# Kernel tuning notes

Measured on AMD Instinct MI355X. Metric: run time of the kernel, lower is better.

The kernel has to match this reference:

```python
import jax, jax.numpy as jnp
import numpy as np

N, CIN, C, L = 6144, 6, 128, 3
SIGMA = 0.3

def _ln(x, g, b, eps=1e-5):
    m = x.mean(-1, keepdims=True)
    v = x.var(-1, keepdims=True)
    return (x - m) / jnp.sqrt(v + eps) * g + b

def _cdist(a):
    n2 = jnp.sum(a * a, -1)
    d2 = n2[:, None] + n2[None, :] - 2.0 * (a @ a.T)
    return jnp.sqrt(jnp.maximum(d2, 0.0))

def setup_inputs():
    key = jax.random.key(0)
    ks = jax.random.split(key, 24)
    s = 1.0 / np.sqrt(C)
    ref = jax.random.normal(ks[0], (N, 3), dtype=jnp.float32)
    src = ref + 0.05 * jax.random.normal(ks[1], (N, 3), dtype=jnp.float32)
    return {
        "ref_keypts": ref,
        "src_keypts": src,
        "corr_feat": jax.random.normal(ks[2], (N, CIN), dtype=jnp.float32),
        "W_in": jax.random.normal(ks[3], (CIN + 6, C), dtype=jnp.float32) * (1.0 / np.sqrt(CIN + 6)),
        "b_in": jnp.zeros((C,), jnp.float32),
        "mlp_W": jax.random.normal(ks[4], (L, C, C), dtype=jnp.float32) * s,
        "mlp_b": jnp.zeros((L, C), jnp.float32),
        "mlp_g": jnp.ones((L, C), jnp.float32),
        "mlp_beta": jnp.zeros((L, C), jnp.float32),
        "Wq": jax.random.normal(ks[5], (L, C, C), dtype=jnp.float32) * s,
        "bq": jnp.zeros((L, C), jnp.float32),
        "Wk": jax.random.normal(ks[6], (L, C, C), dtype=jnp.float32) * s,
        "bk": jnp.zeros((L, C), jnp.float32),
        "Wv": jax.random.normal(ks[7], (L, C, C), dtype=jnp.float32) * s,
        "bv": jnp.zeros((L, C), jnp.float32),
        "Wo": jax.random.normal(ks[8], (L, C, C), dtype=jnp.float32) * s,
        "bo": jnp.zeros((L, C), jnp.float32),
        "ln_g": jnp.ones((L, C), jnp.float32),
        "ln_b": jnp.zeros((L, C), jnp.float32),
        "c1_W": jax.random.normal(ks[9], (C, 32), dtype=jnp.float32) * s,
        "c1_b": jnp.zeros((32,), jnp.float32),
        "c2_W": jax.random.normal(ks[10], (32, 32), dtype=jnp.float32) * (1.0 / np.sqrt(32)),
        "c2_b": jnp.zeros((32,), jnp.float32),
        "c3_W": jax.random.normal(ks[11], (32, 1), dtype=jnp.float32) * (1.0 / np.sqrt(32)),
        "c3_b": jnp.zeros((1,), jnp.float32),
    }

def reference(ref_keypts, src_keypts, corr_feat, W_in, b_in, mlp_W, mlp_b, mlp_g, mlp_beta, Wq, bq, Wk, bk, Wv, bv, Wo, bo, ln_g, ln_b, c1_W, c1_b, c2_W, c2_b, c3_W, c3_b):
    # keypoint-diff embedding
    kp = jnp.concatenate([ref_keypts, src_keypts], -1)          # [N, 6]
    kp = kp - kp.mean(-1, keepdims=True)
    feat = jnp.concatenate([corr_feat, kp], -1) @ W_in + b_in   # [N, C]
    # geometric compatibility (no grad in original -> stop_gradient)
    geo = _cdist(ref_keypts) - _cdist(src_keypts)               # [N, N]
    geo = jnp.maximum(1.0 - geo * geo / (SIGMA * SIGMA), 0.0)
    geo = jax.lax.stop_gradient(geo)
    scale = 1.0 / np.sqrt(C)
    for i in range(L):
        # UnaryBlock: Linear -> norm -> LeakyReLU(0.1)
        h = _ln(feat @ mlp_W[i] + mlp_b[i], mlp_g[i], mlp_beta[i])
        feat = jnp.where(h > 0, h, 0.1 * h)
        # AttentionLayer (1 head) with multiplicative attention_factors
        q = feat @ Wq[i] + bq[i]
        k = feat @ Wk[i] + bk[i]
        v = feat @ Wv[i] + bv[i]
        attn = jax.nn.softmax(geo * ((q @ k.T) * scale), axis=-1)  # [N, N]
        hid = (attn @ v) @ Wo[i] + bo[i]
        feat = _ln(hid + feat, ln_g[i], ln_b[i])
    feat = feat / jnp.maximum(jnp.linalg.norm(feat, axis=-1, keepdims=True), 1e-12)
    h = jax.nn.relu(feat @ c1_W + c1_b)
    h = jax.nn.relu(h @ c2_W + c2_b)
    score = jax.nn.sigmoid(h @ c3_W + c3_b)[:, 0]
    return feat, score
```

## Files before the change

### kernel.cpp

```cpp
#include <hip/hip_runtime.h>
#include <math.h>

#define NPTS 6144
#define CH   128

typedef __attribute__((ext_vector_type(8))) short short8;
typedef __attribute__((ext_vector_type(4))) float f32x4;
typedef __attribute__((ext_vector_type(2))) float f32x2;
typedef __attribute__((ext_vector_type(4))) int   i32x4;
typedef __attribute__((ext_vector_type(2))) int   i32x2;

__device__ inline ushort f2bf(float f) {
  union { float f; unsigned u; } v; v.f = f;
  unsigned u = v.u;
  u += 0x7fff + ((u >> 16) & 1);
  return (ushort)(u >> 16);
}

__device__ inline f32x2 splat2(float x) { return (f32x2){x, x}; }

__device__ inline float fsqrt(float x) {
  float r; asm("v_sqrt_f32 %0, %1" : "=v"(r) : "v"(x)); return r;
}
__device__ inline float fexp2(float x) {
  float r; asm("v_exp_f32 %0, %1" : "=v"(r) : "v"(x)); return r;
}

__global__ __launch_bounds__(128) void k_embed(
    const float* __restrict__ refp, const float* __restrict__ srcp,
    const float* __restrict__ cf, const float* __restrict__ Win,
    const float* __restrict__ bin, float* __restrict__ out) {
  const int row = blockIdx.x, j = threadIdx.x;
  __shared__ float inb[12];
  __shared__ float mkp;
  if (j < 6)       inb[j] = cf[row * 6 + j];
  else if (j < 9)  inb[j] = refp[row * 3 + (j - 6)];
  else if (j < 12) inb[j] = srcp[row * 3 + (j - 9)];
  __syncthreads();
  if (j == 0) {
    float s = inb[6] + inb[7] + inb[8] + inb[9] + inb[10] + inb[11];
    mkp = s * (1.0f / 6.0f);
  }
  __syncthreads();
  float acc = bin[j];
  #pragma unroll
  for (int kk = 0; kk < 12; kk++) {
    float x = inb[kk] - (kk >= 6 ? mkp : 0.0f);
    acc = fmaf(x, Win[kk * CH + j], acc);
  }
  out[row * CH + j] = acc;
}

template <bool RESID, bool LEAKY>
__global__ __launch_bounds__(128) void k_row_linear_ln(
    const float* __restrict__ X, const float* __restrict__ W,
    const float* __restrict__ b, const float* __restrict__ g,
    const float* __restrict__ beta, const float* __restrict__ res,
    float* __restrict__ out) {
  const int j = threadIdx.x;
  const int r0 = blockIdx.x * 4;
  __shared__ float xs[4][CH];
  __shared__ float red[2][4];
  #pragma unroll
  for (int r = 0; r < 4; r++) xs[r][j] = X[(r0 + r) * CH + j];
  __syncthreads();

  float acc[4];
  const float bj = b[j];
  #pragma unroll
  for (int r = 0; r < 4; r++) acc[r] = bj;
  for (int kk = 0; kk < CH; kk++) {
    float w = W[kk * CH + j];
    #pragma unroll
    for (int r = 0; r < 4; r++) acc[r] = fmaf(xs[r][kk], w, acc[r]);
  }
  if (RESID) {
    #pragma unroll
    for (int r = 0; r < 4; r++) acc[r] += res[(r0 + r) * CH + j];
  }

  const int wv = j >> 6, ln = j & 63;
  float sum[4];
  #pragma unroll
  for (int r = 0; r < 4; r++) sum[r] = acc[r];
  #pragma unroll
  for (int o = 32; o; o >>= 1) {
    #pragma unroll
    for (int r = 0; r < 4; r++) sum[r] += __shfl_xor(sum[r], o);
  }
  if (ln == 0) {
    #pragma unroll
    for (int r = 0; r < 4; r++) red[wv][r] = sum[r];
  }
  __syncthreads();
  float mean[4], dv[4];
  #pragma unroll
  for (int r = 0; r < 4; r++) {
    mean[r] = (red[0][r] + red[1][r]) * (1.0f / 128.0f);
    dv[r] = acc[r] - mean[r];
    sum[r] = dv[r] * dv[r];
  }
  #pragma unroll
  for (int o = 32; o; o >>= 1) {
    #pragma unroll
    for (int r = 0; r < 4; r++) sum[r] += __shfl_xor(sum[r], o);
  }
  __syncthreads();
  if (ln == 0) {
    #pragma unroll
    for (int r = 0; r < 4; r++) red[wv][r] = sum[r];
  }
  __syncthreads();
  const float gj = g[j], betaj = beta[j];
  #pragma unroll
  for (int r = 0; r < 4; r++) {
    float var = (red[0][r] + red[1][r]) * (1.0f / 128.0f);
    float y = dv[r] * rsqrtf(var + 1e-5f) * gj + betaj;
    if (LEAKY) y = (y > 0.0f) ? y : 0.1f * y;
    out[(r0 + r) * CH + j] = y;
  }
}

__global__ __launch_bounds__(128) void k_qkv(
    const float* __restrict__ X,
    const float* __restrict__ Wq, const float* __restrict__ bq,
    const float* __restrict__ Wk, const float* __restrict__ bk,
    const float* __restrict__ Wv, const float* __restrict__ bv,
    ushort* __restrict__ Q, ushort* __restrict__ K, ushort* __restrict__ Vt) {
  const int j = threadIdx.x;
  const int r0 = blockIdx.x * 4;
  __shared__ float xs[4][CH];
  #pragma unroll
  for (int r = 0; r < 4; r++) xs[r][j] = X[(r0 + r) * CH + j];
  __syncthreads();
  float aq[4], ak[4], av[4];
  const float bqj = bq[j], bkj = bk[j], bvj = bv[j];
  #pragma unroll
  for (int r = 0; r < 4; r++) { aq[r] = bqj; ak[r] = bkj; av[r] = bvj; }
  for (int kk = 0; kk < CH; kk++) {
    float wq = Wq[kk * CH + j], wk = Wk[kk * CH + j], wv = Wv[kk * CH + j];
    #pragma unroll
    for (int r = 0; r < 4; r++) {
      float x = xs[r][kk];
      aq[r] = fmaf(x, wq, aq[r]);
      ak[r] = fmaf(x, wk, ak[r]);
      av[r] = fmaf(x, wv, av[r]);
    }
  }
  const float scale = 0.12751879524143007f;
  #pragma unroll
  for (int r = 0; r < 4; r++) {
    Q[(r0 + r) * CH + j] = f2bf(aq[r] * scale);
    K[(r0 + r) * CH + j] = f2bf(ak[r]);
  }
  ushort4 vp;
  vp.x = f2bf(av[0]); vp.y = f2bf(av[1]); vp.z = f2bf(av[2]); vp.w = f2bf(av[3]);
  *(ushort4*)(Vt + (size_t)j * NPTS + r0) = vp;
}

__global__ __launch_bounds__(256) void k_attn_mfma(
    const ushort* __restrict__ Q, const ushort* __restrict__ K,
    const ushort* __restrict__ Vt,
    const float* __restrict__ refp, const float* __restrict__ srcp,
    float* __restrict__ Opart, float* __restrict__ ML, int ntiles) {
  const int tid = threadIdx.x;
  const int w = tid >> 6, ln = tid & 63;
  const int l15 = ln & 15, g = ln >> 4;
  const int row0 = blockIdx.x * 64;
  const int seg = blockIdx.y;
  const int t0 = seg * ntiles;

  __shared__ ushort Ks[64 * 128];
  __shared__ ushort Vts[128][72];
  __shared__ float cs2[6][64];

  short8 qf[4];
  {
    const ushort* qp = Q + (size_t)(row0 + 16 * w + l15) * CH + 8 * g;
    #pragma unroll
    for (int ks = 0; ks < 4; ks++) qf[ks] = *(const short8*)(qp + 32 * ks);
  }
  const int qrow = row0 + 16 * w + l15;
  const float rq0 = refp[qrow * 3], rq1 = refp[qrow * 3 + 1], rq2 = refp[qrow * 3 + 2];
  const float sq0 = srcp[qrow * 3], sq1 = srcp[qrow * 3 + 1], sq2 = srcp[qrow * 3 + 2];

  f32x4 oacc[8];
  #pragma unroll
  for (int n = 0; n < 8; n++) oacc[n] = (f32x4){0.f, 0.f, 0.f, 0.f};
  float m = -1e30f, l = 0.0f;
  const float invs2 = 1.0f / (0.3f * 0.3f);

  for (int tt = 0; tt < ntiles; tt++) {
    const int t = t0 + tt;
    __syncthreads();
    #pragma unroll
    for (int s = 0; s < 4; s++) {
      int idx = tid + 256 * s;
      int row = idx >> 4, c8 = idx & 15;
      char* dst = (char*)Ks + row * 256 + ((c8 * 16) ^ ((row & 7) << 4));
      *(short8*)dst = *(const short8*)(K + (size_t)(t * 64 + row) * CH + c8 * 8);
    }
    #pragma unroll
    for (int s = 0; s < 4; s++) {
      int idx = tid + 256 * s;
      int c = idx >> 3, j8 = idx & 7;
      *(short8*)&Vts[c][j8 * 8] =
          *(const short8*)(Vt + (size_t)c * NPTS + t * 64 + j8 * 8);
    }
    if (tid < 64) {
      int gj = t * 64 + tid;
      cs2[0][tid] = refp[gj * 3];     cs2[1][tid] = refp[gj * 3 + 1];
      cs2[2][tid] = refp[gj * 3 + 2]; cs2[3][tid] = srcp[gj * 3];
      cs2[4][tid] = srcp[gj * 3 + 1]; cs2[5][tid] = srcp[gj * 3 + 2];
    }
    __syncthreads();

    f32x4 acc[4];
    #pragma unroll
    for (int nb = 0; nb < 4; nb++) acc[nb] = (f32x4){0.f, 0.f, 0.f, 0.f};
    __builtin_amdgcn_s_setprio(1);
    #pragma unroll
    for (int ks = 0; ks < 4; ks++) {
      #pragma unroll
      for (int nb = 0; nb < 4; nb++) {
        int krow = 16 * nb + l15;
        const char* src = (const char*)Ks + krow * 256 +
                          ((64 * ks + 16 * g) ^ ((krow & 7) << 4));
        short8 af = *(const short8*)src;
        acc[nb] = __builtin_amdgcn_mfma_f32_16x16x32_bf16(af, qf[ks], acc[nb], 0, 0, 0);
      }
    }
    __builtin_amdgcn_s_setprio(0);

    float plog[4][4];
    #pragma unroll
    for (int nb = 0; nb < 4; nb++) {
      const int kb = 16 * nb + 4 * g;
      #pragma unroll
      for (int pp = 0; pp < 2; pp++) {
        const int k2 = kb + 2 * pp;
        f32x2 cx = *(const f32x2*)&cs2[0][k2];
        f32x2 cy = *(const f32x2*)&cs2[1][k2];
        f32x2 cz = *(const f32x2*)&cs2[2][k2];
        f32x2 dx = splat2(rq0) - cx, dy = splat2(rq1) - cy, dz = splat2(rq2) - cz;
        f32x2 d2r = dx * dx + dy * dy + dz * dz;
        cx = *(const f32x2*)&cs2[3][k2];
        cy = *(const f32x2*)&cs2[4][k2];
        cz = *(const f32x2*)&cs2[5][k2];
        dx = splat2(sq0) - cx; dy = splat2(sq1) - cy; dz = splat2(sq2) - cz;
        f32x2 d2s = dx * dx + dy * dy + dz * dz;
        f32x2 prod = d2r * d2s;
        f32x2 sum2 = d2r + d2s;
        float s0 = fsqrt(prod[0]), s1 = fsqrt(prod[1]);
        float dd20 = fmaf(-2.0f, s0, sum2[0]);
        float dd21 = fmaf(-2.0f, s1, sum2[1]);
        float gg0 = fmaxf(fmaf(dd20, -invs2, 1.0f), 0.0f);
        float gg1 = fmaxf(fmaf(dd21, -invs2, 1.0f), 0.0f);
        plog[nb][2 * pp]     = gg0 * acc[nb][2 * pp];
        plog[nb][2 * pp + 1] = gg1 * acc[nb][2 * pp + 1];
      }
    }

    float tm = fmaxf(fmaxf(plog[0][0], plog[0][1]), fmaxf(plog[0][2], plog[0][3]));
    #pragma unroll
    for (int nb = 1; nb < 4; nb++) {
      float t2 = fmaxf(fmaxf(plog[nb][0], plog[nb][1]),
                       fmaxf(plog[nb][2], plog[nb][3]));
      tm = fmaxf(tm, t2);
    }
    tm = fmaxf(tm, __shfl_xor(tm, 16));
    tm = fmaxf(tm, __shfl_xor(tm, 32));
    if (__any(tm > m + 11.0f)) {
      float nm = fmaxf(m, tm);
      float rsc = fexp2(m - nm);
      l *= rsc;
      #pragma unroll
      for (int n = 0; n < 8; n++) oacc[n] *= rsc;
      m = nm;
    }
    float psum = 0.0f;
    #pragma unroll
    for (int nb = 0; nb < 4; nb++)
      #pragma unroll
      for (int r = 0; r < 4; r++) {
        float p = fexp2(plog[nb][r] - m);
        plog[nb][r] = p;
        psum += p;
      }
    psum += __shfl_xor(psum, 16);
    psum += __shfl_xor(psum, 32);
    l += psum;

    unsigned pk[4][2];
    #pragma unroll
    for (int nb = 0; nb < 4; nb++) {
      asm("v_cvt_pk_bf16_f32 %0, %1, %2"
          : "=v"(pk[nb][0]) : "v"(plog[nb][0]), "v"(plog[nb][1]));
      asm("v_cvt_pk_bf16_f32 %0, %1, %2"
          : "=v"(pk[nb][1]) : "v"(plog[nb][2]), "v"(plog[nb][3]));
    }

    union U16 { i32x4 i; short8 s; };
    __builtin_amdgcn_s_setprio(1);
    #pragma unroll
    for (int ks2 = 0; ks2 < 2; ks2++) {
      U16 b;
      b.i[0] = (int)pk[2 * ks2][0];
      b.i[1] = (int)pk[2 * ks2][1];
      b.i[2] = (int)pk[2 * ks2 + 1][0];
      b.i[3] = (int)pk[2 * ks2 + 1][1];
      #pragma unroll
      for (int nb2 = 0; nb2 < 8; nb2++) {
        const ushort* vp2 = &Vts[16 * nb2 + l15][32 * ks2 + 4 * g];
        i32x2 a0 = *(const i32x2*)vp2;
        i32x2 a1 = *(const i32x2*)(vp2 + 16);
        U16 a;
        a.i[0] = a0[0]; a.i[1] = a0[1]; a.i[2] = a1[0]; a.i[3] = a1[1];
        oacc[nb2] = __builtin_amdgcn_mfma_f32_16x16x32_bf16(a.s, b.s, oacc[nb2], 0, 0, 0);
      }
    }
    __builtin_amdgcn_s_setprio(0);
  }

  {
    float* op = Opart + ((size_t)seg * NPTS + qrow) * CH;
    #pragma unroll
    for (int nb2 = 0; nb2 < 8; nb2++)
      *(f32x4*)(op + 16 * nb2 + 4 * g) = oacc[nb2];
    if (g == 0) {
      ML[((size_t)seg * NPTS + qrow) * 2]     = m;
      ML[((size_t)seg * NPTS + qrow) * 2 + 1] = l;
    }
  }
}

__global__ __launch_bounds__(256) void k_attn_combine(
    const float* __restrict__ Opart, const float* __restrict__ ML,
    float* __restrict__ out, int NS) {
  const int tid = threadIdx.x;
  const int row = blockIdx.x * 8 + (tid >> 5);
  const int c4 = (tid & 31) * 4;
  float M = -1e30f;
  for (int s = 0; s < NS; s++)
    M = fmaxf(M, ML[((size_t)s * NPTS + row) * 2]);
  float L = 0.0f;
  f32x4 acc = (f32x4){0.f, 0.f, 0.f, 0.f};
  for (int s = 0; s < NS; s++) {
    float ms = ML[((size_t)s * NPTS + row) * 2];
    float ls = ML[((size_t)s * NPTS + row) * 2 + 1];
    float wsc = fexp2(ms - M);
    L += wsc * ls;
    f32x4 o = *(const f32x4*)&Opart[((size_t)s * NPTS + row) * CH + c4];
    acc[0] = fmaf(wsc, o[0], acc[0]);
    acc[1] = fmaf(wsc, o[1], acc[1]);
    acc[2] = fmaf(wsc, o[2], acc[2]);
    acc[3] = fmaf(wsc, o[3], acc[3]);
  }
  float inv = 1.0f / L;
  f32x4 r = acc * (f32x4){inv, inv, inv, inv};
  *(f32x4*)&out[(size_t)row * CH + c4] = r;
}

__global__ __launch_bounds__(128) void k_final(
    const float* __restrict__ F,
    const float* __restrict__ c1W, const float* __restrict__ c1b,
    const float* __restrict__ c2W, const float* __restrict__ c2b,
    const float* __restrict__ c3W, const float* __restrict__ c3b,
    float* __restrict__ out) {
  const int row = blockIdx.x, j = threadIdx.x;
  __shared__ float xs[CH];
  __shared__ float h1[32];
  __shared__ float h2[32];
  __shared__ float red[2];
  float x = F[row * CH + j];
  float ss = x * x;
  #pragma unroll
  for (int o = 32; o; o >>= 1) ss += __shfl_xor(ss, o);
  if ((j & 63) == 0) red[j >> 6] = ss;
  __syncthreads();
  float norm = sqrtf(red[0] + red[1]);
  float xn = x / fmaxf(norm, 1e-12f);
  xs[j] = xn;
  out[row * CH + j] = xn;
  __syncthreads();
  if (j < 32) {
    float a = c1b[j];
    for (int kk = 0; kk < CH; kk++) a = fmaf(xs[kk], c1W[kk * 32 + j], a);
    h1[j] = fmaxf(a, 0.0f);
  }
  __syncthreads();
  if (j < 32) {
    float a = c2b[j];
    #pragma unroll
    for (int kk = 0; kk < 32; kk++) a = fmaf(h1[kk], c2W[kk * 32 + j], a);
    h2[j] = fmaxf(a, 0.0f);
  }
  __syncthreads();
  if (j == 0) {
    float a = c3b[0];
    #pragma unroll
    for (int kk = 0; kk < 32; kk++) a = fmaf(h2[kk], c3W[kk], a);
    out[NPTS * CH + row] = 1.0f / (1.0f + __expf(-a));
  }
}

extern "C" void kernel_launch(void* const* d_in, const int* in_sizes, int n_in,
                              void* d_out, int out_size, void* d_ws, size_t ws_size,
                              hipStream_t stream) {
  const float* refp = (const float*)d_in[0];
  const float* srcp = (const float*)d_in[1];
  const float* cf   = (const float*)d_in[2];
  const float* Win  = (const float*)d_in[3];
  const float* bin  = (const float*)d_in[4];
  const float* mlpW = (const float*)d_in[5];
  const float* mlpb = (const float*)d_in[6];
  const float* mlpg = (const float*)d_in[7];
  const float* mlpbeta = (const float*)d_in[8];
  const float* Wq = (const float*)d_in[9];
  const float* bq = (const float*)d_in[10];
  const float* Wk = (const float*)d_in[11];
  const float* bk = (const float*)d_in[12];
  const float* Wv = (const float*)d_in[13];
  const float* bv = (const float*)d_in[14];
  const float* Wo = (const float*)d_in[15];
  const float* bo = (const float*)d_in[16];
  const float* lng = (const float*)d_in[17];
  const float* lnb = (const float*)d_in[18];
  const float* c1W = (const float*)d_in[19];
  const float* c1b = (const float*)d_in[20];
  const float* c2W = (const float*)d_in[21];
  const float* c2b = (const float*)d_in[22];
  const float* c3W = (const float*)d_in[23];
  const float* c3b = (const float*)d_in[24];
  float* out = (float*)d_out;

  const size_t NC = (size_t)NPTS * CH;
  float* F = (float*)d_ws;
  float* T = F + NC;
  float* A = T + NC;
  ushort* Qb  = (ushort*)(A + NC);
  ushort* Kb  = Qb + NC;
  ushort* Vtb = Kb + NC;
  float* Opart = (float*)(Vtb + NC);

  const size_t base_bytes = 3 * NC * 4 + 3 * NC * 2;
  int NS = 1;
  for (int cand = 16; cand >= 2; cand >>= 1) {
    size_t need = base_bytes + (size_t)cand * (NC * 4 + NPTS * 8);
    if (need <= ws_size) { NS = cand; break; }
  }
  float* ML = Opart + (size_t)NS * NC;
  const int ntiles = NPTS / 64 / NS;

  k_embed<<<NPTS, 128, 0, stream>>>(refp, srcp, cf, Win, bin, F);
  for (int i = 0; i < 3; i++) {
    const int o2 = i * CH * CH, o1 = i * CH;
    k_row_linear_ln<false, true><<<NPTS / 4, 128, 0, stream>>>(
        F, mlpW + o2, mlpb + o1, mlpg + o1, mlpbeta + o1, nullptr, T);
    k_qkv<<<NPTS / 4, 128, 0, stream>>>(
        T, Wq + o2, bq + o1, Wk + o2, bk + o1, Wv + o2, bv + o1, Qb, Kb, Vtb);
    dim3 agrid(NPTS / 64, NS);
    k_attn_mfma<<<agrid, 256, 0, stream>>>(Qb, Kb, Vtb, refp, srcp, Opart, ML, ntiles);
    k_attn_combine<<<NPTS / 8, 256, 0, stream>>>(Opart, ML, A, NS);
    k_row_linear_ln<true, false><<<NPTS / 4, 128, 0, stream>>>(
        A, Wo + o2, bo + o1, lng + o1, lnb + o1, T, F);
  }
  k_final<<<NPTS, 128, 0, stream>>>(F, c1W, c1b, c2W, c2b, c3W, c3b, out);
}
```

Baseline: 372.2 us.

## Double-buffer K/V tiles via register prefetch and widen attention blocks to 512 threads

The attention kernel now prefetches the next K, V and coordinate tile into registers while computing the current tile, then commits it into a second LDS buffer. This drops one barrier per iteration and hides global-load latency. Blocks grow to 8 waves covering 128 query rows, so each loaded K/V tile is shared by twice as many rows. The XOR swizzle is replaced by padded rows, and V fragments are loaded as a single short8 with a remapped layout. In exchange, register pressure rises from the prefetch registers, and the padding changes the bank-conflict behaviour.

```diff
diff --git a/kernel.cpp b/kernel.cpp
--- a/kernel.cpp
+++ b/kernel.cpp
@@ -158,7 +158,7 @@
   *(ushort4*)(Vt + (size_t)j * NPTS + r0) = vp;
 }
 
-__global__ __launch_bounds__(256) void k_attn_mfma(
+__global__ __launch_bounds__(512, 4) void k_attn_mfma(
     const ushort* __restrict__ Q, const ushort* __restrict__ K,
     const ushort* __restrict__ Vt,
     const float* __restrict__ refp, const float* __restrict__ srcp,
@@ -166,13 +166,53 @@
   const int tid = threadIdx.x;
   const int w = tid >> 6, ln = tid & 63;
   const int l15 = ln & 15, g = ln >> 4;
-  const int row0 = blockIdx.x * 64;
+  const int row0 = blockIdx.x * 128;
   const int seg = blockIdx.y;
   const int t0 = seg * ntiles;
 
-  __shared__ ushort Ks[64 * 128];
-  __shared__ ushort Vts[128][72];
-  __shared__ float cs2[6][64];
+  __shared__ ushort Ks[2][64][136];
+  __shared__ ushort Vs[2][128][72];
+  __shared__ float cs2[2][6][64];
+
+  const int krow0 = tid >> 4;
+  const int kc8   = tid & 15;
+  const int vch0  = tid >> 3;
+  const int vj8   = tid & 7;
+  const int vbase = 32 * (vj8 >> 2) + 4 * (vj8 & 3);
+
+  short8 kreg0, kreg1;
+  i32x2 va0, vb0, va1, vb1;
+  float cr[6];
+
+  auto issue = [&](int t) {
+    const ushort* kp = K + (size_t)(t * 64) * CH + kc8 * 8;
+    kreg0 = *(const short8*)(kp + (size_t)krow0 * CH);
+    kreg1 = *(const short8*)(kp + (size_t)(krow0 + 32) * CH);
+    const ushort* vp0 = Vt + (size_t)vch0 * NPTS + t * 64 + vbase;
+    const ushort* vp1 = vp0 + (size_t)64 * NPTS;
+    va0 = *(const i32x2*)vp0;  vb0 = *(const i32x2*)(vp0 + 16);
+    va1 = *(const i32x2*)vp1;  vb1 = *(const i32x2*)(vp1 + 16);
+    if (tid < 64) {
+      int gj = t * 64 + tid;
+      cr[0] = refp[gj * 3]; cr[1] = refp[gj * 3 + 1]; cr[2] = refp[gj * 3 + 2];
+      cr[3] = srcp[gj * 3]; cr[4] = srcp[gj * 3 + 1]; cr[5] = srcp[gj * 3 + 2];
+    }
+    __builtin_amdgcn_sched_barrier(0);
+  };
+
+  auto commit = [&](int cb) {
+    *(short8*)&Ks[cb][krow0][kc8 * 8] = kreg0;
+    *(short8*)&Ks[cb][krow0 + 32][kc8 * 8] = kreg1;
+    union U16 { i32x4 i; short8 s; } u0, u1;
+    u0.i[0] = va0[0]; u0.i[1] = va0[1]; u0.i[2] = vb0[0]; u0.i[3] = vb0[1];
+    u1.i[0] = va1[0]; u1.i[1] = va1[1]; u1.i[2] = vb1[0]; u1.i[3] = vb1[1];
+    *(short8*)&Vs[cb][vch0][vj8 * 8] = u0.s;
+    *(short8*)&Vs[cb][vch0 + 64][vj8 * 8] = u1.s;
+    if (tid < 64) {
+      #pragma unroll
+      for (int d = 0; d < 6; d++) cs2[cb][d][tid] = cr[d];
+    }
+  };
 
   short8 qf[4];
   {
@@ -190,30 +230,12 @@
   float m = -1e30f, l = 0.0f;
   const float invs2 = 1.0f / (0.3f * 0.3f);
 
+  issue(t0);
+  int cb = 0;
   for (int tt = 0; tt < ntiles; tt++) {
-    const int t = t0 + tt;
+    commit(cb);
     __syncthreads();
-    #pragma unroll
-    for (int s = 0; s < 4; s++) {
-      int idx = tid + 256 * s;
-      int row = idx >> 4, c8 = idx & 15;
-      char* dst = (char*)Ks + row * 256 + ((c8 * 16) ^ ((row & 7) << 4));
-      *(short8*)dst = *(const short8*)(K + (size_t)(t * 64 + row) * CH + c8 * 8);
-    }
-    #pragma unroll
-    for (int s = 0; s < 4; s++) {
-      int idx = tid + 256 * s;
-      int c = idx >> 3, j8 = idx & 7;
-      *(short8*)&Vts[c][j8 * 8] =
-          *(const short8*)(Vt + (size_t)c * NPTS + t * 64 + j8 * 8);
-    }
-    if (tid < 64) {
-      int gj = t * 64 + tid;
-      cs2[0][tid] = refp[gj * 3];     cs2[1][tid] = refp[gj * 3 + 1];
-      cs2[2][tid] = refp[gj * 3 + 2]; cs2[3][tid] = srcp[gj * 3];
-      cs2[4][tid] = srcp[gj * 3 + 1]; cs2[5][tid] = srcp[gj * 3 + 2];
-    }
-    __syncthreads();
+    if (tt + 1 < ntiles) issue(t0 + tt + 1);
 
     f32x4 acc[4];
     #pragma unroll
@@ -223,10 +245,7 @@
     for (int ks = 0; ks < 4; ks++) {
       #pragma unroll
       for (int nb = 0; nb < 4; nb++) {
-        int krow = 16 * nb + l15;
-        const char* src = (const char*)Ks + krow * 256 +
-                          ((64 * ks + 16 * g) ^ ((krow & 7) << 4));
-        short8 af = *(const short8*)src;
+        short8 af = *(const short8*)&Ks[cb][16 * nb + l15][32 * ks + 8 * g];
         acc[nb] = __builtin_amdgcn_mfma_f32_16x16x32_bf16(af, qf[ks], acc[nb], 0, 0, 0);
       }
     }
@@ -239,14 +258,14 @@
       #pragma unroll
       for (int pp = 0; pp < 2; pp++) {
         const int k2 = kb + 2 * pp;
-        f32x2 cx = *(const f32x2*)&cs2[0][k2];
-        f32x2 cy = *(const f32x2*)&cs2[1][k2];
-        f32x2 cz = *(const f32x2*)&cs2[2][k2];
+        f32x2 cx = *(const f32x2*)&cs2[cb][0][k2];
+        f32x2 cy = *(const f32x2*)&cs2[cb][1][k2];
+        f32x2 cz = *(const f32x2*)&cs2[cb][2][k2];
         f32x2 dx = splat2(rq0) - cx, dy = splat2(rq1) - cy, dz = splat2(rq2) - cz;
         f32x2 d2r = dx * dx + dy * dy + dz * dz;
-        cx = *(const f32x2*)&cs2[3][k2];
-        cy = *(const f32x2*)&cs2[4][k2];
-        cz = *(const f32x2*)&cs2[5][k2];
+        cx = *(const f32x2*)&cs2[cb][3][k2];
+        cy = *(const f32x2*)&cs2[cb][4][k2];
+        cz = *(const f32x2*)&cs2[cb][5][k2];
         dx = splat2(sq0) - cx; dy = splat2(sq1) - cy; dz = splat2(sq2) - cz;
         f32x2 d2s = dx * dx + dy * dy + dz * dz;
         f32x2 prod = d2r * d2s;
@@ -311,15 +330,12 @@
       b.i[3] = (int)pk[2 * ks2 + 1][1];
       #pragma unroll
       for (int nb2 = 0; nb2 < 8; nb2++) {
-        const ushort* vp2 = &Vts[16 * nb2 + l15][32 * ks2 + 4 * g];
-        i32x2 a0 = *(const i32x2*)vp2;
-        i32x2 a1 = *(const i32x2*)(vp2 + 16);
-        U16 a;
-        a.i[0] = a0[0]; a.i[1] = a0[1]; a.i[2] = a1[0]; a.i[3] = a1[1];
-        oacc[nb2] = __builtin_amdgcn_mfma_f32_16x16x32_bf16(a.s, b.s, oacc[nb2], 0, 0, 0);
+        short8 vf = *(const short8*)&Vs[cb][16 * nb2 + l15][32 * ks2 + 8 * g];
+        oacc[nb2] = __builtin_amdgcn_mfma_f32_16x16x32_bf16(vf, b.s, oacc[nb2], 0, 0, 0);
       }
     }
     __builtin_amdgcn_s_setprio(0);
+    cb ^= 1;
   }
 
   {
@@ -459,8 +475,8 @@
         F, mlpW + o2, mlpb + o1, mlpg + o1, mlpbeta + o1, nullptr, T);
     k_qkv<<<NPTS / 4, 128, 0, stream>>>(
         T, Wq + o2, bq + o1, Wk + o2, bk + o1, Wv + o2, bv + o1, Qb, Kb, Vtb);
-    dim3 agrid(NPTS / 64, NS);
-    k_attn_mfma<<<agrid, 256, 0, stream>>>(Qb, Kb, Vtb, refp, srcp, Opart, ML, ntiles);
+    dim3 agrid(NPTS / 128, NS);
+    k_attn_mfma<<<agrid, 512, 0, stream>>>(Qb, Kb, Vtb, refp, srcp, Opart, ML, ntiles);
     k_attn_combine<<<NPTS / 8, 256, 0, stream>>>(Opart, ML, A, NS);
     k_row_linear_ln<true, false><<<NPTS / 4, 128, 0, stream>>>(
         A, Wo + o2, bo + o1, lng + o1, lnb + o1, T, F);
```

New measurement: 353.0 us. -5.2%, faster.
